# Kernel optimization log

Hardware: AMD Instinct MI355X
Metric: run time of the kernel (lower is better)

Reference implementation:

```python
import jax, jax.numpy as jnp
import numpy as np

D_MODEL = 1024
HEAD_SIZE = 64
BLOCK_SIZE = 2048
B, T = 4, 2048


def setup_inputs() -> dict:
    key = jax.random.key(0)
    ks = jax.random.split(key, 7)
    s = 1.0 / np.sqrt(D_MODEL)
    x = jax.random.normal(ks[0], (B, T, D_MODEL), dtype=jnp.float32)
    Wq = jax.random.uniform(ks[1], (D_MODEL, HEAD_SIZE), jnp.float32, -s, s)
    bq = jax.random.uniform(ks[2], (HEAD_SIZE,), jnp.float32, -s, s)
    Wk = jax.random.uniform(ks[3], (D_MODEL, HEAD_SIZE), jnp.float32, -s, s)
    bk = jax.random.uniform(ks[4], (HEAD_SIZE,), jnp.float32, -s, s)
    Wv = jax.random.uniform(ks[5], (D_MODEL, HEAD_SIZE), jnp.float32, -s, s)
    return {"x": x, "Wq": Wq, "bq": bq, "Wk": Wk, "bk": bk, "Wv": Wv, "mask": 1}


def reference(x, Wq, bq, Wk, bk, Wv, mask):
    # x: [B, T, C]; single attention head, dropout is identity (eval/p=0)
    Tlen = x.shape[1]
    q = x @ Wq + bq              # [B, T, hs]
    k = x @ Wk + bk              # [B, T, hs]
    v = x @ Wv                   # [B, T, hs] (no bias)
    hs = k.shape[-1]
    # Faithful to source: weights = QK^T / hs**(-0.5)  ==  QK^T * sqrt(hs)
    w = jnp.einsum('btd,bsd->bts', q, k) * jnp.sqrt(jnp.asarray(hs, x.dtype))
    if mask:
        causal = jnp.tril(jnp.ones((Tlen, Tlen), dtype=bool))
        w = jnp.where(causal, w, jnp.asarray(-jnp.inf, w.dtype))
    w = jax.nn.softmax(w, axis=-1)
    out = jnp.einsum('bts,bsd->btd', w, v)  # [B, T, hs]
    return out
```

## Files before the change

### kernel.cpp

```cpp
#include <hip/hip_runtime.h>
#include <hip/hip_bf16.h>

#define D_MODEL 1024
#define HS 64
#define T_LEN 2048
#define JCH 512
#define NCH 4

typedef __attribute__((ext_vector_type(8))) short bf16x8;
typedef __attribute__((ext_vector_type(4))) float f32x4;

__device__ inline void split8(const float* v, int4& hi, int4& lo) {
    union { unsigned short u[8]; int4 v4; } uh, ul;
    #pragma unroll
    for (int i = 0; i < 8; ++i) {
        const unsigned int b = __float_as_uint(v[i]);
        const unsigned short h = (unsigned short)(b >> 16);
        const float r = v[i] - __uint_as_float((unsigned int)h << 16);
        uh.u[i] = h;
        ul.u[i] = (unsigned short)(__float_as_uint(r) >> 16);
    }
    hi = uh.v4; lo = ul.v4;
}

__device__ inline unsigned short f2bf_rne(float f) {
    const unsigned int b = __float_as_uint(f);
    return (unsigned short)((b + 0x7FFFu + ((b >> 16) & 1u)) >> 16);
}
__device__ inline float bf2f(unsigned short h) {
    return __uint_as_float((unsigned int)h << 16);
}

__device__ inline void async_copy16(const short* g, short* l) {
    __builtin_amdgcn_global_load_lds(
        (const __attribute__((address_space(1))) void*)g,
        (__attribute__((address_space(3))) void*)l, 16, 0, 0);
}

__global__ __launch_bounds__(256) void prep_kernel(
    const float* __restrict__ x,
    const float* __restrict__ Wq, const float* __restrict__ Wk,
    const float* __restrict__ Wv,
    short* __restrict__ xh, short* __restrict__ xl,
    short* __restrict__ wh, short* __restrict__ wl, int BT)
{
    __shared__ float tile[64][69];
    const int tid = threadIdx.x;
    const int bx  = blockIdx.x;
    const int nxb = BT >> 4;

    if (bx < nxb) {
        const int mtg = bx;
        #pragma unroll
        for (int i = 0; i < 8; ++i) {
            const int s    = tid + 256 * i;
            const int kc   = s >> 6;
            const int lane = s & 63;
            const float* src = x + (size_t)(mtg * 16 + (lane & 15)) * D_MODEL
                                 + kc * 32 + (lane >> 4) * 8;
            float v[8];
            *(float4*)&v[0] = *(const float4*)src;
            *(float4*)&v[4] = *(const float4*)(src + 4);
            int4 hi, lo;
            split8(v, hi, lo);
            const size_t off = ((size_t)(mtg * 32 + kc) * 64 + lane) * 8;
            *(int4*)(xh + off) = hi;
            *(int4*)(xl + off) = lo;
        }
    } else {
        const int wb = bx - nxb;
        const int kb = wb & 15;
        const int m  = wb >> 4;
        const float* W = (m == 0) ? Wq : (m == 1) ? Wk : Wv;
        #pragma unroll
        for (int it = 0; it < 4; ++it) {
            const int idx = tid + 256 * it;
            const int kr = idx >> 4, c4 = idx & 15;
            *(float4*)&tile[kr][4 * c4] =
                *(const float4*)(W + (size_t)(kb * 64 + kr) * HS + 4 * c4);
        }
        __syncthreads();
        #pragma unroll
        for (int i = 0; i < 2; ++i) {
            const int s    = tid + 256 * i;
            const int ntl  = s >> 7;
            const int kcl  = (s >> 6) & 1;
            const int lane = s & 63;
            const int n    = ntl * 16 + (lane & 15);
            const int krel = kcl * 32 + (lane >> 4) * 8;
            float v[8];
            #pragma unroll
            for (int e = 0; e < 8; ++e) v[e] = tile[krel + e][n];
            int4 hi, lo;
            split8(v, hi, lo);
            const size_t off =
                ((size_t)((m * 4 + ntl) * 32 + kb * 2 + kcl) * 64 + lane) * 8;
            *(int4*)(wh + off) = hi;
            *(int4*)(wl + off) = lo;
        }
    }
}

__global__ __launch_bounds__(256) void qkv_kernel(
    const short* __restrict__ xh, const short* __restrict__ xl,
    const short* __restrict__ wh, const short* __restrict__ wl,
    const float* __restrict__ bq, const float* __restrict__ bk,
    float* __restrict__ q, float* __restrict__ k, float* __restrict__ vt, int BT)
{
    __shared__ __align__(16) short A_lds[8 * 512];
    __shared__ __align__(16) short B_lds[16 * 512];

    const int tid  = threadIdx.x;
    const int r0   = blockIdx.x * 32;
    const int nb   = blockIdx.y;
    const int wave = tid >> 6;
    const int lane = tid & 63;
    const int mt_w = wave >> 1;
    const int nt0  = (wave & 1) * 2;

    f32x4 acc0 = (f32x4)(0.f);
    f32x4 acc1 = (f32x4)(0.f);

    const size_t mtg0 = (size_t)(r0 >> 4);
    const size_t ntg0 = (size_t)(nb * 4);

    for (int k0 = 0; k0 < D_MODEL; k0 += 64) {
        const int kc0 = k0 >> 5;
        __syncthreads();
        #pragma unroll
        for (int ii = 0; ii < 6; ++ii) {
            const int g = wave * 6 + ii;
            if (g < 8) {
                const int mt = g >> 2, kcl = (g >> 1) & 1, p = g & 1;
                const short* base = p ? xl : xh;
                const short* gsrc = base + ((mtg0 + mt) * 32 + kc0 + kcl) * 512;
                async_copy16(gsrc + lane * 8, &A_lds[g * 512]);
            } else {
                const int gb = g - 8;
                const int nt = gb >> 2, kcl = (gb >> 1) & 1, p = gb & 1;
                const short* base = p ? wl : wh;
                const short* gsrc = base + ((ntg0 + nt) * 32 + kc0 + kcl) * 512;
                async_copy16(gsrc + lane * 8, &B_lds[gb * 512]);
            }
        }
        __syncthreads();
        #pragma unroll
        for (int kcl = 0; kcl < 2; ++kcl) {
            const bf16x8 afh = *(const bf16x8*)&A_lds[(mt_w * 4 + kcl * 2 + 0) * 512 + lane * 8];
            const bf16x8 afl = *(const bf16x8*)&A_lds[(mt_w * 4 + kcl * 2 + 1) * 512 + lane * 8];
            {
                const bf16x8 bfh = *(const bf16x8*)&B_lds[(nt0 * 4 + kcl * 2 + 0) * 512 + lane * 8];
                const bf16x8 bfl = *(const bf16x8*)&B_lds[(nt0 * 4 + kcl * 2 + 1) * 512 + lane * 8];
                acc0 = __builtin_amdgcn_mfma_f32_16x16x32_bf16(afh, bfh, acc0, 0, 0, 0);
                acc0 = __builtin_amdgcn_mfma_f32_16x16x32_bf16(afh, bfl, acc0, 0, 0, 0);
                acc0 = __builtin_amdgcn_mfma_f32_16x16x32_bf16(afl, bfh, acc0, 0, 0, 0);
            }
            {
                const bf16x8 bfh = *(const bf16x8*)&B_lds[((nt0 + 1) * 4 + kcl * 2 + 0) * 512 + lane * 8];
                const bf16x8 bfl = *(const bf16x8*)&B_lds[((nt0 + 1) * 4 + kcl * 2 + 1) * 512 + lane * 8];
                acc1 = __builtin_amdgcn_mfma_f32_16x16x32_bf16(afh, bfh, acc1, 0, 0, 0);
                acc1 = __builtin_amdgcn_mfma_f32_16x16x32_bf16(afh, bfl, acc1, 0, 0, 0);
                acc1 = __builtin_amdgcn_mfma_f32_16x16x32_bf16(afl, bfh, acc1, 0, 0, 0);
            }
        }
    }

    const int rowb = r0 + mt_w * 16 + (lane >> 4) * 4;
    #pragma unroll
    for (int j = 0; j < 2; ++j) {
        const f32x4 a = (j == 0) ? acc0 : acc1;
        const int c = nb * 64 + (nt0 + j) * 16 + (lane & 15);
        if (c < 64) {
            const float bias = bq[c];
            #pragma unroll
            for (int r = 0; r < 4; ++r)
                q[(size_t)(rowb + r) * HS + c] = a[r] + bias;
        } else if (c < 128) {
            const float bias = bk[c - 64];
            #pragma unroll
            for (int r = 0; r < 4; ++r)
                k[(size_t)(rowb + r) * HS + (c - 64)] = a[r] + bias;
        } else {
            float4 o;
            o.x = a[0]; o.y = a[1]; o.z = a[2]; o.w = a[3];
            *(float4*)(vt + (size_t)(c - 128) * BT + rowb) = o;
        }
    }
}

__global__ __launch_bounds__(256) void kvprep_kernel(
    const float* __restrict__ k, const float* __restrict__ vt,
    short* __restrict__ kfh, short* __restrict__ kfl, short* __restrict__ vf,
    int BT)
{
    const int tid = threadIdx.x;
    const int bx  = blockIdx.x;
    const int nkb = BT >> 6;

    if (bx < nkb) {
        #pragma unroll
        for (int i = 0; i < 2; ++i) {
            const int s    = tid + 256 * i;
            const int tl   = s >> 7;
            const int kc   = (s >> 6) & 1;
            const int lane = s & 63;
            const int row  = bx * 64 + tl * 16 + (lane & 15);
            const int col  = kc * 32 + (lane >> 4) * 8;
            const float* src = k + (size_t)row * HS + col;
            float v[8];
            *(float4*)&v[0] = *(const float4*)src;
            *(float4*)&v[4] = *(const float4*)(src + 4);
            int4 hi, lo;
            split8(v, hi, lo);
            const size_t off = (((size_t)(bx * 4 + tl) * 2 + kc) * 64 + lane) * 8;
            *(int4*)(kfh + off) = hi;
            *(int4*)(kfl + off) = lo;
        }
    } else {
        const int vb = bx - nkb;
        #pragma unroll
        for (int i = 0; i < 2; ++i) {
            const int s    = tid + 256 * i;
            const int gg   = s >> 6;
            const int lane = s & 63;
            const int n    = (gg & 3) * 16 + (lane & 15);
            const int j    = vb * 64 + (gg >> 2) * 32 + (lane >> 4) * 8;
            const float* src = vt + (size_t)n * BT + j;
            float v[8];
            *(float4*)&v[0] = *(const float4*)src;
            *(float4*)&v[4] = *(const float4*)(src + 4);
            union { unsigned short u[8]; int4 i4; } pk;
            #pragma unroll
            for (int e = 0; e < 8; ++e) pk.u[e] = f2bf_rne(v[e]);
            *(int4*)(vf + ((size_t)(vb * 8 + gg) * 64 + lane) * 8) = pk.i4;
        }
    }
}

__global__ __launch_bounds__(256) void attn_kernel(
    const float* __restrict__ q_ws,
    const short* __restrict__ kfh, const short* __restrict__ kfl,
    const short* __restrict__ vf, const int* __restrict__ maskp,
    float* __restrict__ part_O, float* __restrict__ part_ml, int BT)
{
    __shared__ __align__(16) short Kh[4096], Kl[4096];
    __shared__ __align__(16) short Vt[4096];
    __shared__ __align__(16) short Pl[4][16 * 72];

    const int tile  = blockIdx.x;
    const int chunk = blockIdx.y;
    const int r0 = tile * 64;
    const int tb = r0 / T_LEN;
    const int t0 = r0 - tb * T_LEN;
    const int mask = (*maskp != 0);
    const int n_max = mask ? (t0 + 64) : T_LEN;
    const int j0 = chunk * JCH;
    if (j0 >= n_max) return;
    const int hi_j = min(j0 + JCH, n_max);
    const int njt = (hi_j - j0 + 63) >> 6;

    const int tid  = threadIdx.x;
    const int w    = tid >> 6;
    const int lane = tid & 63;
    const int quad = lane >> 4;
    const int l15  = lane & 15;
    const int rw0  = t0 + 16 * w;
    const int rowa = r0 + 16 * w + quad * 4;

    bf16x8 qfh[2], qfl[2];
    {
        const float* qrow = q_ws + (size_t)(r0 + 16 * w + l15) * HS + quad * 8;
        #pragma unroll
        for (int kc = 0; kc < 2; ++kc) {
            float v[8];
            *(float4*)&v[0] = *(const float4*)(qrow + kc * 32);
            *(float4*)&v[4] = *(const float4*)(qrow + kc * 32 + 4);
            union { int4 i; bf16x8 b; } ch, cl;
            split8(v, ch.i, cl.i);
            qfh[kc] = ch.b;
            qfl[kc] = cl.b;
        }
    }

    f32x4 oacc[4];
    #pragma unroll
    for (int nt = 0; nt < 4; ++nt) oacc[nt] = (f32x4)(0.f);
    float m_r[4] = {-INFINITY, -INFINITY, -INFINITY, -INFINITY};
    float l_r[4] = {0.f, 0.f, 0.f, 0.f};

    for (int jt = 0; jt < njt; ++jt) {
        const int jbase = j0 + jt * 64;
        __syncthreads();
        {
            const size_t kt0 = (size_t)(tb * 128) + (jbase >> 4);
            const size_t vb  = (size_t)(tb * 32) + (jbase >> 6);
            #pragma unroll
            for (int ii = 0; ii < 6; ++ii) {
                const int g = w * 6 + ii;
                if (g < 8) {
                    const short* src = kfh + ((kt0 + (g >> 1)) * 2 + (g & 1)) * 512;
                    async_copy16(src + lane * 8, &Kh[g * 512]);
                } else if (g < 16) {
                    const int gg = g - 8;
                    const short* src = kfl + ((kt0 + (gg >> 1)) * 2 + (gg & 1)) * 512;
                    async_copy16(src + lane * 8, &Kl[gg * 512]);
                } else {
                    const int gg = g - 16;
                    const short* src = vf + (vb * 8 + gg) * 512;
                    async_copy16(src + lane * 8, &Vt[gg * 512]);
                }
            }
        }
        __syncthreads();

        const bool active = (!mask) || (jbase <= rw0 + 15);
        if (active) {
            f32x4 sacc[4];
            #pragma unroll
            for (int jsub = 0; jsub < 4; ++jsub) {
                f32x4 s = (f32x4)(0.f);
                #pragma unroll
                for (int kc = 0; kc < 2; ++kc) {
                    const bf16x8 kh = *(const bf16x8*)&Kh[((jsub * 2 + kc) * 64 + lane) * 8];
                    const bf16x8 kl = *(const bf16x8*)&Kl[((jsub * 2 + kc) * 64 + lane) * 8];
                    s = __builtin_amdgcn_mfma_f32_16x16x32_bf16(qfh[kc], kh, s, 0, 0, 0);
                    s = __builtin_amdgcn_mfma_f32_16x16x32_bf16(qfh[kc], kl, s, 0, 0, 0);
                    s = __builtin_amdgcn_mfma_f32_16x16x32_bf16(qfl[kc], kh, s, 0, 0, 0);
                }
                sacc[jsub] = s;
            }
            float sval[4][4], rmax[4];
            #pragma unroll
            for (int r = 0; r < 4; ++r) rmax[r] = -INFINITY;
            #pragma unroll
            for (int jsub = 0; jsub < 4; ++jsub) {
                const int jg = jbase + jsub * 16 + l15;
                #pragma unroll
                for (int r = 0; r < 4; ++r) {
                    const int tg = rw0 + quad * 4 + r;
                    const float vv = (mask && (jg > tg)) ? -INFINITY : 8.0f * sacc[jsub][r];
                    sval[jsub][r] = vv;
                    rmax[r] = fmaxf(rmax[r], vv);
                }
            }
            #pragma unroll
            for (int d = 1; d < 16; d <<= 1)
                #pragma unroll
                for (int r = 0; r < 4; ++r)
                    rmax[r] = fmaxf(rmax[r], __shfl_xor(rmax[r], d));
            float alpha[4], msafe[4];
            #pragma unroll
            for (int r = 0; r < 4; ++r) {
                const float mn = fmaxf(m_r[r], rmax[r]);
                msafe[r] = (mn == -INFINITY) ? 0.f : mn;
                alpha[r] = __expf(m_r[r] - msafe[r]);
                m_r[r] = mn;
            }
            short* Pw = &Pl[w][0];
            float rsum[4] = {0.f, 0.f, 0.f, 0.f};
            #pragma unroll
            for (int jsub = 0; jsub < 4; ++jsub) {
                #pragma unroll
                for (int r = 0; r < 4; ++r) {
                    const float e = __expf(sval[jsub][r] - msafe[r]);
                    const unsigned short eb = f2bf_rne(e);
                    Pw[(quad * 4 + r) * 72 + jsub * 16 + l15] = (short)eb;
                    rsum[r] += bf2f(eb);
                }
            }
            #pragma unroll
            for (int d = 1; d < 16; d <<= 1)
                #pragma unroll
                for (int r = 0; r < 4; ++r)
                    rsum[r] += __shfl_xor(rsum[r], d);
            #pragma unroll
            for (int r = 0; r < 4; ++r)
                l_r[r] = l_r[r] * alpha[r] + rsum[r];
            #pragma unroll
            for (int nt = 0; nt < 4; ++nt)
                #pragma unroll
                for (int r = 0; r < 4; ++r)
                    oacc[nt][r] *= alpha[r];
            bf16x8 pf[2];
            #pragma unroll
            for (int jc = 0; jc < 2; ++jc)
                pf[jc] = *(const bf16x8*)&Pw[l15 * 72 + jc * 32 + quad * 8];
            #pragma unroll
            for (int nt = 0; nt < 4; ++nt) {
                #pragma unroll
                for (int jc = 0; jc < 2; ++jc) {
                    const bf16x8 vfr = *(const bf16x8*)&Vt[((jc * 4 + nt) * 64 + lane) * 8];
                    oacc[nt] = __builtin_amdgcn_mfma_f32_16x16x32_bf16(pf[jc], vfr, oacc[nt], 0, 0, 0);
                }
            }
        }
    }

    #pragma unroll
    for (int nt = 0; nt < 4; ++nt)
        #pragma unroll
        for (int r = 0; r < 4; ++r)
            part_O[((size_t)(rowa + r) * NCH + chunk) * HS + nt * 16 + l15] = oacc[nt][r];
    if (l15 == 0) {
        #pragma unroll
        for (int r = 0; r < 4; ++r) {
            float2 ml;
            ml.x = m_r[r];
            ml.y = l_r[r];
            *(float2*)(part_ml + ((size_t)(rowa + r) * NCH + chunk) * 2) = ml;
        }
    }
}

__global__ __launch_bounds__(256) void combine_kernel(
    const float* __restrict__ part_O, const float* __restrict__ part_ml,
    const int* __restrict__ maskp, float* __restrict__ out)
{
    const int f = blockIdx.x * 256 + threadIdx.x;
    const int row = f >> 6;
    const int d = f & 63;
    const int t = row & (T_LEN - 1);
    const int mask = (*maskp != 0);
    const int n = mask ? (t + 1) : T_LEN;
    const int nc = (n + JCH - 1) / JCH;

    const float2* mlp = (const float2*)(part_ml + (size_t)row * NCH * 2);
    float M = -INFINITY;
    for (int c = 0; c < nc; ++c) M = fmaxf(M, mlp[c].x);
    float L = 0.f, O = 0.f;
    for (int c = 0; c < nc; ++c) {
        const float2 ml = mlp[c];
        const float w = __expf(ml.x - M);
        L += ml.y * w;
        O = fmaf(part_O[((size_t)row * NCH + c) * HS + d], w, O);
    }
    out[(size_t)row * HS + d] = O / L;
}

extern "C" void kernel_launch(void* const* d_in, const int* in_sizes, int n_in,
                              void* d_out, int out_size, void* d_ws, size_t ws_size,
                              hipStream_t stream) {
    const float* x  = (const float*)d_in[0];
    const float* Wq = (const float*)d_in[1];
    const float* bq = (const float*)d_in[2];
    const float* Wk = (const float*)d_in[3];
    const float* bk = (const float*)d_in[4];
    const float* Wv = (const float*)d_in[5];
    const int* maskp = (const int*)d_in[6];

    const int BT = in_sizes[0] / D_MODEL;

    float* q   = (float*)d_ws;
    float* k   = q + (size_t)BT * HS;
    float* vt  = k + (size_t)BT * HS;
    float* pO  = vt + (size_t)BT * HS;
    float* pml = pO + (size_t)BT * NCH * HS;
    short* xh  = (short*)(pml + (size_t)BT * NCH * 2);
    short* xl  = xh + (size_t)BT * D_MODEL;
    short* wh  = xl + (size_t)BT * D_MODEL;
    short* wl  = wh + (size_t)192 * D_MODEL;
    short* kfh = wl + (size_t)192 * D_MODEL;
    short* kfl = kfh + (size_t)BT * HS;
    short* vf  = kfl + (size_t)BT * HS;

    prep_kernel<<<BT / 16 + 48, 256, 0, stream>>>(x, Wq, Wk, Wv, xh, xl, wh, wl, BT);
    dim3 qgrid(BT / 32, 3);
    qkv_kernel<<<qgrid, 256, 0, stream>>>(xh, xl, wh, wl, bq, bk, q, k, vt, BT);
    kvprep_kernel<<<BT / 32, 256, 0, stream>>>(k, vt, kfh, kfl, vf, BT);
    dim3 agrid(BT / 64, NCH);
    attn_kernel<<<agrid, 256, 0, stream>>>(q, kfh, kfl, vf, maskp, pO, pml, BT);
    combine_kernel<<<(BT * HS) / 256, 256, 0, stream>>>(pO, pml, maskp, (float*)d_out);
}
```

Before: 140.3 us.

## Fuse K/V fragment packing into QKV epilogue and double attention key chunks

The QKV GEMM epilogue now writes K directly as split bf16 hi/lo MFMA fragments and V as rounded bf16 fragments, which removes the separate kvprep kernel and the fp32 K/V round trip through global memory. The attention split is also changed from 4 chunks of 512 keys to 8 chunks of 256, raising the number of attention blocks at the cost of larger partial buffers and more combine work. The fused epilogue uses scattered 2-byte stores for K, which may coalesce poorly.

```diff
diff --git a/kernel.cpp b/kernel.cpp
--- a/kernel.cpp
+++ b/kernel.cpp
@@ -4,8 +4,8 @@
 #define D_MODEL 1024
 #define HS 64
 #define T_LEN 2048
-#define JCH 512
-#define NCH 4
+#define JCH 256
+#define NCH 8
 
 typedef __attribute__((ext_vector_type(8))) short bf16x8;
 typedef __attribute__((ext_vector_type(4))) float f32x4;
@@ -105,7 +105,9 @@
     const short* __restrict__ xh, const short* __restrict__ xl,
     const short* __restrict__ wh, const short* __restrict__ wl,
     const float* __restrict__ bq, const float* __restrict__ bk,
-    float* __restrict__ q, float* __restrict__ k, float* __restrict__ vt, int BT)
+    float* __restrict__ q,
+    short* __restrict__ kfh, short* __restrict__ kfl, short* __restrict__ vf,
+    int BT)
 {
     __shared__ __align__(16) short A_lds[8 * 512];
     __shared__ __align__(16) short B_lds[16 * 512];
@@ -176,63 +178,38 @@
             for (int r = 0; r < 4; ++r)
                 q[(size_t)(rowb + r) * HS + c] = a[r] + bias;
         } else if (c < 128) {
-            const float bias = bk[c - 64];
-            #pragma unroll
-            for (int r = 0; r < 4; ++r)
-                k[(size_t)(rowb + r) * HS + (c - 64)] = a[r] + bias;
+            const int ck    = c - 64;
+            const float bias = bk[ck];
+            const int ktile = rowb >> 4;
+            const int kc2   = ck >> 5;
+            const int quadd = (ck & 31) >> 3;
+            const int e     = ck & 7;
+            #pragma unroll
+            for (int r = 0; r < 4; ++r) {
+                const float val = a[r] + bias;
+                const unsigned int b = __float_as_uint(val);
+                const unsigned short h = (unsigned short)(b >> 16);
+                const float res = val - __uint_as_float((unsigned int)h << 16);
+                const unsigned short l16 = (unsigned short)(__float_as_uint(res) >> 16);
+                const int laned = ((rowb + r) & 15) | (quadd << 4);
+                const size_t off = ((size_t)((ktile * 2 + kc2) * 64 + laned)) * 8 + e;
+                kfh[off] = (short)h;
+                kfl[off] = (short)l16;
+            }
         } else {
-            float4 o;
-            o.x = a[0]; o.y = a[1]; o.z = a[2]; o.w = a[3];
-            *(float4*)(vt + (size_t)(c - 128) * BT + rowb) = o;
-        }
-    }
-}
-
-__global__ __launch_bounds__(256) void kvprep_kernel(
-    const float* __restrict__ k, const float* __restrict__ vt,
-    short* __restrict__ kfh, short* __restrict__ kfl, short* __restrict__ vf,
-    int BT)
-{
-    const int tid = threadIdx.x;
-    const int bx  = blockIdx.x;
-    const int nkb = BT >> 6;
-
-    if (bx < nkb) {
-        #pragma unroll
-        for (int i = 0; i < 2; ++i) {
-            const int s    = tid + 256 * i;
-            const int tl   = s >> 7;
-            const int kc   = (s >> 6) & 1;
-            const int lane = s & 63;
-            const int row  = bx * 64 + tl * 16 + (lane & 15);
-            const int col  = kc * 32 + (lane >> 4) * 8;
-            const float* src = k + (size_t)row * HS + col;
-            float v[8];
-            *(float4*)&v[0] = *(const float4*)src;
-            *(float4*)&v[4] = *(const float4*)(src + 4);
-            int4 hi, lo;
-            split8(v, hi, lo);
-            const size_t off = (((size_t)(bx * 4 + tl) * 2 + kc) * 64 + lane) * 8;
-            *(int4*)(kfh + off) = hi;
-            *(int4*)(kfl + off) = lo;
-        }
-    } else {
-        const int vb = bx - nkb;
-        #pragma unroll
-        for (int i = 0; i < 2; ++i) {
-            const int s    = tid + 256 * i;
-            const int gg   = s >> 6;
-            const int lane = s & 63;
-            const int n    = (gg & 3) * 16 + (lane & 15);
-            const int j    = vb * 64 + (gg >> 2) * 32 + (lane >> 4) * 8;
-            const float* src = vt + (size_t)n * BT + j;
-            float v[8];
-            *(float4*)&v[0] = *(const float4*)src;
-            *(float4*)&v[4] = *(const float4*)(src + 4);
-            union { unsigned short u[8]; int4 i4; } pk;
-            #pragma unroll
-            for (int e = 0; e < 8; ++e) pk.u[e] = f2bf_rne(v[e]);
-            *(int4*)(vf + ((size_t)(vb * 8 + gg) * 64 + lane) * 8) = pk.i4;
+            const int cv    = c - 128;
+            const int vb    = rowb >> 6;
+            const int jc2   = (rowb & 63) >> 5;
+            const int quadd = (rowb & 31) >> 3;
+            const int gg    = jc2 * 4 + (cv >> 4);
+            const int laned = (cv & 15) | (quadd << 4);
+            const size_t base = ((size_t)((vb * 8 + gg) * 64 + laned)) * 8 + (rowb & 7);
+            short4 pk;
+            pk.x = (short)f2bf_rne(a[0]);
+            pk.y = (short)f2bf_rne(a[1]);
+            pk.z = (short)f2bf_rne(a[2]);
+            pk.w = (short)f2bf_rne(a[3]);
+            *(short4*)(vf + base) = pk;
         }
     }
 }
@@ -451,9 +428,7 @@
     const int BT = in_sizes[0] / D_MODEL;
 
     float* q   = (float*)d_ws;
-    float* k   = q + (size_t)BT * HS;
-    float* vt  = k + (size_t)BT * HS;
-    float* pO  = vt + (size_t)BT * HS;
+    float* pO  = q + (size_t)BT * HS;
     float* pml = pO + (size_t)BT * NCH * HS;
     short* xh  = (short*)(pml + (size_t)BT * NCH * 2);
     short* xl  = xh + (size_t)BT * D_MODEL;
@@ -465,8 +440,7 @@
 
     prep_kernel<<<BT / 16 + 48, 256, 0, stream>>>(x, Wq, Wk, Wv, xh, xl, wh, wl, BT);
     dim3 qgrid(BT / 32, 3);
-    qkv_kernel<<<qgrid, 256, 0, stream>>>(xh, xl, wh, wl, bq, bk, q, k, vt, BT);
-    kvprep_kernel<<<BT / 32, 256, 0, stream>>>(k, vt, kfh, kfl, vf, BT);
+    qkv_kernel<<<qgrid, 256, 0, stream>>>(xh, xl, wh, wl, bq, bk, q, kfh, kfl, vf, BT);
     dim3 agrid(BT / 64, NCH);
     attn_kernel<<<agrid, 256, 0, stream>>>(q, kfh, kfl, vf, maskp, pO, pml, BT);
     combine_kernel<<<(BT * HS) / 256, 256, 0, stream>>>(pO, pml, maskp, (float*)d_out);
```

New measurement: 137.9 us. No clear change (-1.7%).
